# Kernel optimization log

Hardware: AMD Instinct MI355X
Metric: run time of the kernel (lower is better)

Reference implementation:

```python
import jax, jax.numpy as jnp
import numpy as np

N_WIN = 7      # regions per side (BiFormer nchw BRA default)
TOPK = 4       # routed regions per query region
NH = 1         # num_heads (RefNet_encoder uses num_heads=1)
EPS = 1e-5


def _resize(x, hw):
    n, c = x.shape[:2]
    # torch F.interpolate(mode='bilinear', align_corners=False)
    return jax.image.resize(x, (n, c, hw[0], hw[1]), method='bilinear', antialias=False)


def _conv1x1(x, w, b):
    return jnp.einsum('nchw,oc->nohw', x, w) + b[None, :, None, None]


def _ln2d(x, g, b):
    # LayerNorm over channel dim of NCHW
    mu = jnp.mean(x, axis=1, keepdims=True)
    var = jnp.var(x, axis=1, keepdims=True)
    return (x - mu) * jax.lax.rsqrt(var + EPS) * g[None, :, None, None] + b[None, :, None, None]


def _to_regions(t, nh):
    # (N,C,H,W) -> (N, nh, R, rs, hd) with R = n_win^2 regions, rs tokens/region
    n, c, h, w = t.shape
    hd = c // nh
    rh, rw = h // N_WIN, w // N_WIN
    t = t.reshape(n, nh, hd, N_WIN, rh, N_WIN, rw)
    return t.transpose(0, 1, 3, 5, 4, 6, 2).reshape(n, nh, N_WIN * N_WIN, rh * rw, hd)


def _from_regions(t, h, w):
    n, nh, _, _, hd = t.shape
    rh, rw = h // N_WIN, w // N_WIN
    t = t.reshape(n, nh, N_WIN, N_WIN, rh, rw, hd)
    return t.transpose(0, 1, 6, 2, 4, 3, 5).reshape(n, nh * hd, h, w)


def _dwconv(x, w, b):
    # depthwise 5x5 LePE conv, padding=2
    y = jax.lax.conv_general_dilated(x, w, (1, 1), 'SAME',
        dimension_numbers=('NCHW', 'OIHW', 'NCHW'), feature_group_count=x.shape[1])
    return y + b[None, :, None, None]


def _bra(x, mask, qkv_w, qkv_b, lepe_w, lepe_b, proj_w, proj_b):
    n, c, h, w = x.shape
    hd = c // NH
    scale = hd ** -0.5
    rh, rw = h // N_WIN, w // N_WIN
    rs = rh * rw
    R = N_WIN * N_WIN
    q, k, v = jnp.split(_conv1x1(x, qkv_w, qkv_b), 3, axis=1)
    # region-to-region routing graph on detached q/k (avg-pooled regions)
    qd = jax.lax.stop_gradient(q).reshape(n, c, N_WIN, rh, N_WIN, rw).mean(axis=(3, 5)).reshape(n, c, R)
    kd = jax.lax.stop_gradient(k).reshape(n, c, N_WIN, rh, N_WIN, rw).mean(axis=(3, 5)).reshape(n, c, R)
    a_r = jnp.einsum('ncp,ncq->npq', qd, kd)             # (n, R, R)
    idx = jax.lax.top_k(a_r, TOPK)[1]                     # (n, R, TOPK)
    # token-to-token attention within routed regions
    qr = _to_regions(q, NH)                               # (n, nh, R, rs, hd)
    kr = _to_regions(k, NH)
    vr = _to_regions(v, NH)
    gidx = idx[:, None, :, :, None, None]                 # (n,1,Rq,topk,1,1)
    kg = jnp.take_along_axis(kr[:, :, None], gidx, axis=3).reshape(n, NH, R, TOPK * rs, hd)
    vg = jnp.take_along_axis(vr[:, :, None], gidx, axis=3).reshape(n, NH, R, TOPK * rs, hd)
    attn = jnp.einsum('nhrqd,nhrkd->nhrqk', qr * scale, kg)
    # glass-mask additive bias, partitioned + gathered exactly like the keys
    mr = _to_regions(mask, 1)[..., 0]                     # (n,1,R,rs)
    mg = jnp.take_along_axis(mr[:, :, None], idx[:, None, :, :, None], axis=3)
    attn = attn + mg.reshape(n, 1, R, 1, TOPK * rs)
    attn = jax.nn.softmax(attn, axis=-1)
    out = jnp.einsum('nhrqk,nhrkd->nhrqd', attn, vg)
    out = _from_regions(out, h, w) + _dwconv(v, lepe_w, lepe_b)
    return _conv1x1(out, proj_w, proj_b)


def _block(x, mask, i, ln1_g, ln1_b, ln2_g, ln2_b, qkv_w, qkv_b, lepe_w, lepe_b,
           proj_w, proj_b, fc1_w, fc1_b, fc2_w, fc2_b):
    x = x + _bra(_ln2d(x, ln1_g[i], ln1_b[i]), mask, qkv_w[i], qkv_b[i],
                 lepe_w[i], lepe_b[i], proj_w[i], proj_b[i])
    h = jax.nn.gelu(_conv1x1(_ln2d(x, ln2_g[i], ln2_b[i]), fc1_w[i], fc1_b[i]), approximate=False)
    return x + _conv1x1(h, fc2_w[i], fc2_b[i])


def reference(exemplar0, exemplar, input1, exemplar_pre, conv0_w, conv0_b,
              ln1_g, ln1_b, ln2_g, ln2_b, qkv_w, qkv_b, lepe_w, lepe_b,
              proj_w, proj_b, fc1_w, fc1_b, fc2_w, fc2_b):
    hw = exemplar.shape[2:]
    pre_s = _resize(exemplar_pre, hw)
    feats_s = _resize(exemplar0, hw)
    img_s = _resize(input1, hw)
    x = jnp.concatenate([feats_s, exemplar, img_s], axis=1)
    hx = jax.lax.conv_general_dilated(x, conv0_w, (1, 1), 'SAME',
        dimension_numbers=('NCHW', 'OIHW', 'NCHW')) + conv0_b[None, :, None, None]
    m = (jax.nn.sigmoid(pre_s) > 0.5).astype(x.dtype)
    attn_mask = jnp.where(m == 0, jnp.float32(-100.0), jnp.float32(0.0)).astype(x.dtype)
    for i in range(4):
        hx = _block(hx, attn_mask, i, ln1_g, ln1_b, ln2_g, ln2_b, qkv_w, qkv_b,
                    lepe_w, lepe_b, proj_w, proj_b, fc1_w, fc1_b, fc2_w, fc2_b)
    return hx


def setup_inputs() -> dict:
    key = jax.random.key(0)
    ks = jax.random.split(key, 12)
    B, C, H, W = 4, 64, 112, 112
    s = 0.05
    return {
        'exemplar0': jax.random.normal(ks[0], (B, C, 224, 224), jnp.float32),
        'exemplar': jax.random.normal(ks[1], (B, C, H, W), jnp.float32),
        'input1': jax.random.normal(ks[2], (B, 3, 224, 224), jnp.float32),
        'exemplar_pre': jax.random.normal(ks[3], (B, 1, 224, 224), jnp.float32),
        'conv0_w': jax.random.normal(ks[4], (C, 2 * C + 3, 3, 3), jnp.float32) * s,
        'conv0_b': jnp.zeros((C,), jnp.float32),
        'ln1_g': jnp.ones((4, C), jnp.float32),
        'ln1_b': jnp.zeros((4, C), jnp.float32),
        'ln2_g': jnp.ones((4, C), jnp.float32),
        'ln2_b': jnp.zeros((4, C), jnp.float32),
        'qkv_w': jax.random.normal(ks[5], (4, 3 * C, C), jnp.float32) * s,
        'qkv_b': jnp.zeros((4, 3 * C), jnp.float32),
        'lepe_w': jax.random.normal(ks[6], (4, C, 1, 5, 5), jnp.float32) * s,
        'lepe_b': jnp.zeros((4, C), jnp.float32),
        'proj_w': jax.random.normal(ks[7], (4, C, C), jnp.float32) * s,
        'proj_b': jnp.zeros((4, C), jnp.float32),
        'fc1_w': jax.random.normal(ks[8], (4, 4 * C, C), jnp.float32) * s,
        'fc1_b': jnp.zeros((4, 4 * C), jnp.float32),
        'fc2_w': jax.random.normal(ks[9], (4, C, 4 * C), jnp.float32) * s,
        'fc2_b': jnp.zeros((4, C), jnp.float32),
    }
```

## Files before the change

### kernel.cpp

```cpp
#include <hip/hip_runtime.h>

#define HW 112
#define PP 12544
#define BB 4
#define RR 49
#define RS 256
#define GW 114
#define GP (GW*GW)
#define CK 160

typedef __bf16 bf16;
typedef __bf16 bf16x8 __attribute__((ext_vector_type(8)));
typedef __bf16 bf16x4 __attribute__((ext_vector_type(4)));
typedef float f32x4 __attribute__((ext_vector_type(4)));

__device__ __forceinline__ int swzg(int row, int halfcol, int rowbytes) {
  int byte = halfcol * 2;
  return row * rowbytes + (byte & ~127) + ((((byte >> 4) ^ row) & 7) * 16) + (byte & 15);
}
__device__ __forceinline__ int swz128(int row, int halfcol) { return swzg(row, halfcol, 128); }

__device__ __forceinline__ float gelu_exact(float x) {
  return 0.5f * x * (1.f + erff(x * 0.70710678118654752f));
}

__device__ __forceinline__ void gl_lds16(const void* g, void* l) {
  __builtin_amdgcn_global_load_lds((const __attribute__((address_space(1))) unsigned int*)g,
                                   (__attribute__((address_space(3))) unsigned int*)l, 16, 0, 0);
}
__device__ __forceinline__ void gl_lds4(const void* g, void* l) {
  __builtin_amdgcn_global_load_lds((const __attribute__((address_space(1))) unsigned int*)g,
                                   (__attribute__((address_space(3))) unsigned int*)l, 4, 0, 0);
}

__global__ __launch_bounds__(256) void k_prep2(const float* __restrict__ ex0, const float* __restrict__ ex,
    const float* __restrict__ img, const float* __restrict__ pre,
    bf16* __restrict__ xct, float* __restrict__ maskr) {
  __shared__ bf16 sT2[64 * 168];
  int n = blockIdx.y;
  int p0 = blockIdx.x * 64;
  int tid = threadIdx.x;
  uint4 zz = {0, 0, 0, 0};
  for (int i2 = tid; i2 < 1344; i2 += 256) ((uint4*)sT2)[i2] = zz;
  __syncthreads();
  int l = tid & 63, g = tid >> 6;
  int p = p0 + l;
  int h = p / HW, w = p % HW;
  for (int c = g; c < 131; c += 4) {
    float val;
    if (c < 64) {
      const float* s = ex0 + (((size_t)(n * 64 + c)) * 224 + 2 * h) * 224 + 2 * w;
      val = 0.5f * (0.5f * (s[0] + s[224]) + 0.5f * (s[1] + s[225]));
    } else if (c < 128) {
      val = ex[((size_t)(n * 64 + (c - 64))) * PP + p];
    } else {
      const float* s = img + (((size_t)(n * 3 + (c - 128))) * 224 + 2 * h) * 224 + 2 * w;
      val = 0.5f * (0.5f * (s[0] + s[224]) + 0.5f * (s[1] + s[225]));
    }
    sT2[l * 168 + c] = (bf16)val;
  }
  if (tid < 64) {
    const float* s = pre + ((size_t)n * 224 + 2 * h) * 224 + 2 * w;
    float v = 0.5f * (0.5f * (s[0] + s[224]) + 0.5f * (s[1] + s[225]));
    int r = (h >> 4) * 7 + (w >> 4); int sIdx = (h & 15) * 16 + (w & 15);
    maskr[(n * RR + r) * RS + sIdx] = (v > 0.0f) ? 0.0f : -100.0f;
  }
  __syncthreads();
  for (int i2 = tid; i2 < 1280; i2 += 256) {
    int row = i2 / 20, ch = i2 % 20;
    int pr = p0 + row;
    int hh = pr / HW, ww = pr % HW;
    uint4 d = *(const uint4*)(sT2 + row * 168 + ch * 8);
    *(uint4*)(xct + ((size_t)n * GP + (hh + 1) * GW + ww + 1) * CK + ch * 8) = d;
  }
}

__global__ __launch_bounds__(256) void k_wt2(const float* __restrict__ w, bf16* __restrict__ wTb) {
  int t = blockIdx.x * 256 + threadIdx.x;
  if (t >= 9 * 5 * 64 * 32) return;
  int cc = t & 31; int o = (t >> 5) & 63; int ks = (t >> 11) % 5; int k = t / 10240;
  int c = ks * 32 + cc;
  wTb[t] = (bf16)((c < 131) ? w[((size_t)(o * 131) + c) * 9 + k] : 0.f);
}

__global__ __launch_bounds__(256) void k_conv0m(const bf16* __restrict__ xct, const bf16* __restrict__ wTb,
    const float* __restrict__ bias, float* __restrict__ out_t) {
  __shared__ bf16 sA[128 * 32];
  __shared__ bf16 sB[64 * 32];
  int n = blockIdx.y;
  int p0 = blockIdx.x * 128;
  int tid = threadIdx.x, lane = tid & 63, wv = tid >> 6;
  int lo = lane & 15, hi = lane >> 4;
  size_t gofsA[2];
  #pragma unroll
  for (int it = 0; it < 2; it++) {
    int idx = tid + it * 256;
    int row = idx >> 2, ch = idx & 3;
    int p = p0 + row;
    int hh = p / HW, ww = p % HW;
    gofsA[it] = ((size_t)(hh + 1) * GW + ww + 1) * (CK * 2) + ch * 16;
  }
  const char* xbase = (const char*)(xct + (size_t)n * GP * CK);
  f32x4 acc[2][4];
  #pragma unroll
  for (int mi = 0; mi < 2; mi++)
    #pragma unroll
    for (int ni = 0; ni < 4; ni++) acc[mi][ni] = (f32x4){0.f, 0.f, 0.f, 0.f};
  for (int tap = 0; tap < 9; tap++) {
    long shift = (long)((tap / 3 - 1) * GW + (tap % 3 - 1)) * (CK * 2);
    for (int ks = 0; ks < 5; ks++) {
      uint4 a0 = *(const uint4*)(xbase + gofsA[0] + shift + ks * 64);
      uint4 a1 = *(const uint4*)(xbase + gofsA[1] + shift + ks * 64);
      uint4 b0 = *(const uint4*)((const char*)wTb + ((size_t)(tap * 5 + ks) * 2048 + tid * 8) * 2);
      __syncthreads();
      *(uint4*)((char*)sA + tid * 16) = a0;
      *(uint4*)((char*)sA + (tid + 256) * 16) = a1;
      *(uint4*)((char*)sB + tid * 16) = b0;
      __syncthreads();
      bf16x8 aF[2], bF[4];
      #pragma unroll
      for (int mi = 0; mi < 2; mi++)
        aF[mi] = *(const bf16x8*)((const char*)sA + (wv * 32 + mi * 16 + lo) * 64 + hi * 16);
      #pragma unroll
      for (int ni = 0; ni < 4; ni++)
        bF[ni] = *(const bf16x8*)((const char*)sB + (ni * 16 + lo) * 64 + hi * 16);
      #pragma unroll
      for (int mi = 0; mi < 2; mi++)
        #pragma unroll
        for (int ni = 0; ni < 4; ni++)
          acc[mi][ni] = __builtin_amdgcn_mfma_f32_16x16x32_bf16(aF[mi], bF[ni], acc[mi][ni], 0, 0, 0);
    }
  }
  #pragma unroll
  for (int ni = 0; ni < 4; ni++) {
    float bv = bias[ni * 16 + lo];
    #pragma unroll
    for (int mi = 0; mi < 2; mi++) {
      #pragma unroll
      for (int r2 = 0; r2 < 4; r2++) {
        int p = p0 + wv * 32 + mi * 16 + hi * 4 + r2;
        out_t[((size_t)n * PP + p) * 64 + ni * 16 + lo] = acc[mi][ni][r2] + bv;
      }
    }
  }
}

__global__ __launch_bounds__(256) void k_qkvr(const float* __restrict__ xin, const float* __restrict__ lng,
    const float* __restrict__ lnb, const float* __restrict__ w, const float* __restrict__ bias,
    bf16* __restrict__ qRo, bf16* __restrict__ kRo, bf16* __restrict__ vto, bf16* __restrict__ vTo,
    float* __restrict__ qd, float* __restrict__ kd) {
  __shared__ __align__(16) char smem[43008];
  bf16* sA = (bf16*)smem;
  bf16* sB = (bf16*)(smem + 32768);
  float* rq = (float*)(smem + 40960);
  float* rk = (float*)(smem + 41984);
  bf16* sT = (bf16*)smem;
  int r = blockIdx.x, n = blockIdx.y;
  int nr = n * RR + r;
  int rh = (r / 7) * 16, rw = (r % 7) * 16;
  int tid = threadIdx.x, lane = tid & 63, wv = tid >> 6;
  int lo = lane & 15, hi = lane >> 4;
  #pragma unroll
  for (int h2 = 0; h2 < 2; h2++) {
    int row = h2 * 128 + (tid >> 1), part = tid & 1;
    int y = row >> 4, x = row & 15;
    const float* xp = xin + ((size_t)n * PP + (rh + y) * HW + rw + x) * 64 + part * 32;
    float v[32]; float s = 0.f, sq = 0.f;
    #pragma unroll
    for (int i = 0; i < 8; i++) {
      float4 d = *(const float4*)&xp[i * 4];
      v[i*4]=d.x; v[i*4+1]=d.y; v[i*4+2]=d.z; v[i*4+3]=d.w;
      s += d.x+d.y+d.z+d.w;
      sq += d.x*d.x+d.y*d.y+d.z*d.z+d.w*d.w;
    }
    s += __shfl_xor(s, 1, 64); sq += __shfl_xor(sq, 1, 64);
    float mu = s * (1.f/64.f);
    float rstd = rsqrtf(fmaxf(sq * (1.f/64.f) - mu*mu, 0.f) + 1e-5f);
    #pragma unroll
    for (int j2 = 0; j2 < 4; j2++) {
      bf16x8 o8;
      #pragma unroll
      for (int e = 0; e < 8; e++) {
        int c = part*32 + j2*8 + e;
        o8[e] = (bf16)((v[j2*8+e] - mu) * rstd * lng[c] + lnb[c]);
      }
      *(bf16x8*)((char*)sA + swz128(row, part*32 + j2*8)) = o8;
    }
  }
  for (int ob = 0; ob < 3; ob++) {
    #pragma unroll
    for (int it = 0; it < 4; it++) {
      int idx = tid + it * 256;
      int oo = idx >> 4, q = idx & 15;
      float4 wv4 = *(const float4*)&w[(size_t)(ob * 64 + oo) * 64 + q * 4];
      bf16x4 b4; b4[0] = (bf16)wv4.x; b4[1] = (bf16)wv4.y; b4[2] = (bf16)wv4.z; b4[3] = (bf16)wv4.w;
      *(bf16x4*)((char*)sB + swz128(oo, q * 4)) = b4;
    }
    __syncthreads();
    f32x4 acc[4][4];
    #pragma unroll
    for (int mi = 0; mi < 4; mi++)
      #pragma unroll
      for (int ni = 0; ni < 4; ni++) acc[mi][ni] = (f32x4){0.f, 0.f, 0.f, 0.f};
    #pragma unroll
    for (int kk = 0; kk < 2; kk++) {
      bf16x8 aF[4], bF[4];
      #pragma unroll
      for (int mi = 0; mi < 4; mi++)
        aF[mi] = *(const bf16x8*)((const char*)sA + swz128(wv * 64 + mi * 16 + lo, kk * 32 + hi * 8));
      #pragma unroll
      for (int ni = 0; ni < 4; ni++)
        bF[ni] = *(const bf16x8*)((const char*)sB + swz128(ni * 16 + lo, kk * 32 + hi * 8));
      #pragma unroll
      for (int mi = 0; mi < 4; mi++)
        #pragma unroll
        for (int ni = 0; ni < 4; ni++)
          acc[mi][ni] = __builtin_amdgcn_mfma_f32_16x16x32_bf16(aF[mi], bF[ni], acc[mi][ni], 0, 0, 0);
    }
    float bv[4];
    #pragma unroll
    for (int ni = 0; ni < 4; ni++) bv[ni] = bias[ob * 64 + ni * 16 + lo];
    if (ob == 0) {
      float part_[4] = {0.f, 0.f, 0.f, 0.f};
      #pragma unroll
      for (int ni = 0; ni < 4; ni++) {
        #pragma unroll
        for (int mi = 0; mi < 4; mi++) {
          #pragma unroll
          for (int r2 = 0; r2 < 4; r2++) {
            float rv = acc[mi][ni][r2] + bv[ni];
            int s = wv * 64 + mi * 16 + hi * 4 + r2;
            qRo[((size_t)nr * RS + s) * 64 + ni * 16 + lo] = (bf16)(rv * 0.125f);
            part_[ni] += rv;
          }
        }
        part_[ni] += __shfl_xor(part_[ni], 16, 64);
        part_[ni] += __shfl_xor(part_[ni], 32, 64);
        if (hi == 0) rq[wv * 64 + ni * 16 + lo] = part_[ni];
      }
      __syncthreads();
    } else if (ob == 1) {
      float part_[4] = {0.f, 0.f, 0.f, 0.f};
      #pragma unroll
      for (int ni = 0; ni < 4; ni++) {
        #pragma unroll
        for (int mi = 0; mi < 4; mi++) {
          #pragma unroll
          for (int r2 = 0; r2 < 4; r2++) {
            float rv = acc[mi][ni][r2] + bv[ni];
            int s = wv * 64 + mi * 16 + hi * 4 + r2;
            kRo[((size_t)nr * RS + s) * 64 + ni * 16 + lo] = (bf16)rv;
            part_[ni] += rv;
          }
        }
        part_[ni] += __shfl_xor(part_[ni], 16, 64);
        part_[ni] += __shfl_xor(part_[ni], 32, 64);
        if (hi == 0) rk[wv * 64 + ni * 16 + lo] = part_[ni];
      }
      __syncthreads();
    } else {
      __syncthreads();
      #pragma unroll
      for (int ni = 0; ni < 4; ni++) {
        int ch = ni * 16 + lo;
        #pragma unroll
        for (int mi = 0; mi < 4; mi++) {
          #pragma unroll
          for (int r2 = 0; r2 < 4; r2++) {
            float rv = acc[mi][ni][r2] + bv[ni];
            int s = wv * 64 + mi * 16 + hi * 4 + r2;
            bf16 b = (bf16)rv;
            vto[((size_t)n * PP + (rh + (s >> 4)) * HW + rw + (s & 15)) * 64 + ch] = b;
            sT[ch * 264 + s] = b;
          }
        }
      }
      __syncthreads();
      #pragma unroll
      for (int it = 0; it < 8; it++) {
        int idx = tid + it * 256;
        int row = idx >> 5, ch8 = idx & 31;
        uint4 d = *(const uint4*)(sT + row * 264 + ch8 * 8);
        *(uint4*)(vTo + ((size_t)nr * 64 + row) * 256 + ch8 * 8) = d;
      }
      if (tid < 64) {
        int c = tid;
        qd[(n * 64 + c) * RR + r] = ((rq[c] + rq[64 + c]) + (rq[128 + c] + rq[192 + c])) * (1.f / 256.f);
        kd[(n * 64 + c) * RR + r] = ((rk[c] + rk[64 + c]) + (rk[128 + c] + rk[192 + c])) * (1.f / 256.f);
      }
    }
  }
}

__global__ __launch_bounds__(64) void k_topk(const float* __restrict__ qd, const float* __restrict__ kd,
    int* __restrict__ gidx) {
  int pq = blockIdx.x, n = blockIdx.y;
  int j = threadIdx.x;
  float a = -3e38f;
  if (j < RR) {
    a = 0.f;
    for (int c = 0; c < 64; c++)
      a += qd[(n * 64 + c) * RR + pq] * kd[(n * 64 + c) * RR + j];
  }
  for (int t = 0; t < 4; t++) {
    float bv = a; int bj = j;
    #pragma unroll
    for (int d = 32; d >= 1; d >>= 1) {
      float ov = __shfl_xor(bv, d, 64);
      int oj = __shfl_xor(bj, d, 64);
      if (ov > bv || (ov == bv && oj < bj)) { bv = ov; bj = oj; }
    }
    if (j == 0) gidx[(n * RR + pq) * 4 + t] = bj;
    if (j == bj) a = -3e38f;
  }
}

__global__ __launch_bounds__(512, 6) void k_attn(const bf16* __restrict__ qR, const bf16* __restrict__ kR,
    const bf16* __restrict__ vT, const float* __restrict__ maskr, const int* __restrict__ gidx,
    bf16* __restrict__ attnRb) {
  __shared__ bf16 sKd[2][64 * 64];
  __shared__ bf16 sVd[2][64 * 64];
  __shared__ bf16 sP[8][16 * 64];
  __shared__ float sMaskB[2][64];
  int bid = blockIdx.x;
  int newid = (bid & 7) * 49 + (bid >> 3);
  int n = newid / (RR * 2); int rem = newid % (RR * 2); int r = rem >> 1, qsp = rem & 1;
  int tid = threadIdx.x, lane = tid & 63, wv = tid >> 6;
  int lo = lane & 15, hi = lane >> 4;
  int m0 = qsp * 128 + wv * 16;
  const bf16* qbase = qR + ((size_t)(n * RR + r)) * RS * 64;
  bf16x8 qF[2];
  #pragma unroll
  for (int kk = 0; kk < 2; kk++)
    qF[kk] = *(const bf16x8*)(qbase + (m0 + lo) * 64 + kk * 32 + hi * 8);

  int gofsK, gofsV;
  {
    int rowT = wv * 8 + (lane >> 3);
    int c4 = ((lane & 7) ^ rowT) & 7;
    gofsK = rowT * 128 + c4 * 16;
    gofsV = rowT * 512 + c4 * 16;
  }

  const int* gptr = gidx + (n * RR + r) * 4;
  int j0g = gptr[0], j1g = gptr[1], j2g = gptr[2], j3g = gptr[3];

  f32x4 zero4 = {0.f, 0.f, 0.f, 0.f};
  f32x4 Oacc[4];
  #pragma unroll
  for (int di = 0; di < 4; di++) Oacc[di] = zero4;
  float mrun = -3e38f, lrun = 0.f;

  #define ISSUE_TILE(JREG, SUB, BUF) do {                                            \
    const char* kb_ = (const char*)(kR + ((size_t)(n * RR + (JREG))) * RS * 64) + (SUB) * 8192; \
    const char* vb_ = (const char*)(vT + ((size_t)(n * RR + (JREG))) * 64 * RS) + (SUB) * 128;  \
    gl_lds16(kb_ + gofsK, (char*)sKd + (BUF) * 8192 + wv * 1024);                    \
    gl_lds16(vb_ + gofsV, (char*)sVd + (BUF) * 8192 + wv * 1024);                    \
    if (wv == 0) gl_lds4(maskr + ((size_t)(n * RR + (JREG))) * RS + (SUB) * 64 + lane, (char*)sMaskB[(BUF)]); \
  } while (0)

  ISSUE_TILE(j0g, 0, 0);

  for (int ts = 0; ts < 16; ts++) {
    int cur = ts & 1;
    asm volatile("s_waitcnt lgkmcnt(0)" ::: "memory");
    __builtin_amdgcn_s_barrier();
    __builtin_amdgcn_sched_barrier(0);
    if (ts < 15) {
      int nts = ts + 1;
      int jn = (nts < 8) ? (nts < 4 ? j0g : j1g) : (nts < 12 ? j2g : j3g);
      int nsub = nts & 3;
      ISSUE_TILE(jn, nsub, cur ^ 1);
      if (wv == 0) { asm volatile("s_waitcnt vmcnt(3)" ::: "memory"); }
      else         { asm volatile("s_waitcnt vmcnt(2)" ::: "memory"); }
    } else {
      asm volatile("s_waitcnt vmcnt(0)" ::: "memory");
    }
    __builtin_amdgcn_s_barrier();
    __builtin_amdgcn_sched_barrier(0);
    const char* sK = (const char*)sKd + cur * 8192;
    const char* sV = (const char*)sVd + cur * 8192;
    f32x4 Sacc[4];
    #pragma unroll
    for (int ni = 0; ni < 4; ni++) Sacc[ni] = zero4;
    #pragma unroll
    for (int kk = 0; kk < 2; kk++) {
      #pragma unroll
      for (int ni = 0; ni < 4; ni++) {
        bf16x8 kF = *(const bf16x8*)(sK + swz128(ni * 16 + lo, kk * 32 + hi * 8));
        Sacc[ni] = __builtin_amdgcn_mfma_f32_16x16x32_bf16(kF, qF[kk], Sacc[ni], 0, 0, 0);
      }
    }
    const float* mB = sMaskB[cur];
    float ml = -3e38f;
    #pragma unroll
    for (int ni = 0; ni < 4; ni++) {
      #pragma unroll
      for (int jj = 0; jj < 4; jj++) {
        float sv = Sacc[ni][jj] + mB[ni * 16 + hi * 4 + jj];
        Sacc[ni][jj] = sv;
        ml = fmaxf(ml, sv);
      }
    }
    ml = fmaxf(ml, __shfl_xor(ml, 16, 64));
    ml = fmaxf(ml, __shfl_xor(ml, 32, 64));
    float nm = fmaxf(mrun, ml);
    float sc = __expf(mrun - nm);
    float rs = 0.f;
    bf16* sPw = sP[wv];
    #pragma unroll
    for (int ni = 0; ni < 4; ni++) {
      #pragma unroll
      for (int jj = 0; jj < 4; jj++) {
        float pv = __expf(Sacc[ni][jj] - nm);
        rs += pv;
        *(bf16*)((char*)sPw + swz128(lo, ni * 16 + hi * 4 + jj)) = (bf16)pv;
      }
    }
    rs += __shfl_xor(rs, 16, 64);
    rs += __shfl_xor(rs, 32, 64);
    mrun = nm; lrun = lrun * sc + rs;
    float scq[4];
    #pragma unroll
    for (int jj = 0; jj < 4; jj++) scq[jj] = __shfl(sc, hi * 4 + jj, 16);
    #pragma unroll
    for (int di = 0; di < 4; di++)
      #pragma unroll
      for (int jj = 0; jj < 4; jj++) Oacc[di][jj] *= scq[jj];
    #pragma unroll
    for (int kk = 0; kk < 2; kk++) {
      bf16x8 pF = *(const bf16x8*)((const char*)sPw + swz128(lo, kk * 32 + hi * 8));
      #pragma unroll
      for (int di = 0; di < 4; di++) {
        bf16x8 vF = *(const bf16x8*)(sV + swz128(di * 16 + lo, kk * 32 + hi * 8));
        Oacc[di] = __builtin_amdgcn_mfma_f32_16x16x32_bf16(pF, vF, Oacc[di], 0, 0, 0);
      }
    }
  }
  #undef ISSUE_TILE
  __syncthreads();
  float inv = 1.f / lrun;
  float invq[4];
  #pragma unroll
  for (int jj = 0; jj < 4; jj++) invq[jj] = __shfl(inv, hi * 4 + jj, 16);
  bf16* sOut = (bf16*)sKd;
  #pragma unroll
  for (int jj = 0; jj < 4; jj++) {
    int row = wv * 16 + hi * 4 + jj;
    #pragma unroll
    for (int di = 0; di < 4; di++)
      sOut[row * 64 + di * 16 + lo] = (bf16)(Oacc[di][jj] * invq[jj]);
  }
  __syncthreads();
  bf16* dst = attnRb + (((size_t)(n * RR + r)) * RS + qsp * 128) * 64;
  #pragma unroll
  for (int it = 0; it < 2; it++) {
    int idx = tid + it * 512;
    *(uint4*)(dst + idx * 8) = *(const uint4*)(sOut + idx * 8);
  }
}

__global__ __launch_bounds__(256) void k_lepe3(const bf16* __restrict__ v_t, const bf16* __restrict__ attnRb,
    const float* __restrict__ lw, const float* __restrict__ lb,
    const float* __restrict__ pw, const float* __restrict__ pb, float* __restrict__ xo) {
  __shared__ __align__(16) char smem[64000];
  bf16* sH = (bf16*)smem;
  float* sW = (float*)(smem + 57600);
  bf16* zA = (bf16*)smem;
  bf16* sBp = (bf16*)(smem + 32768);
  int r = blockIdx.x, n = blockIdx.y;
  int rh = (r / 7) * 16, rw = (r % 7) * 16;
  int tid = threadIdx.x, lane = tid & 63, wv = tid >> 6;
  int lo = lane & 15, hi = lane >> 4;
  for (int i = tid; i < 1600; i += 256) { int c = i / 25, k = i % 25; sW[k * 64 + c] = lw[c * 25 + k]; }
  for (int g = tid; g < 3200; g += 256) {
    int pix = g >> 3, c4 = g & 7;
    int yy = pix / 20, xx = pix % 20;
    int hh = rh + yy - 2, ww = rw + xx - 2;
    uint4 d = {0, 0, 0, 0};
    if ((unsigned)hh < HW && (unsigned)ww < HW)
      d = *(const uint4*)(v_t + ((size_t)n * PP + hh * HW + ww) * 64 + c4 * 8);
    *(uint4*)((char*)sH + pix * 144 + c4 * 16) = d;
  }
  __syncthreads();
  int y = tid >> 4, x = tid & 15;
  float acc[64];
  const bf16* ar = attnRb + (((size_t)(n * RR + r)) * RS + tid) * 64;
  #pragma unroll
  for (int c8 = 0; c8 < 8; c8++) {
    bf16x8 av = *(const bf16x8*)(ar + c8 * 8);
    #pragma unroll
    for (int j = 0; j < 8; j++) acc[c8 * 8 + j] = lb[c8 * 8 + j] + (float)av[j];
  }
  for (int t25 = 0; t25 < 25; t25++) {
    int dh = t25 / 5, dw = t25 % 5;
    int pix = (y + dh) * 20 + (x + dw);
    #pragma unroll
    for (int c8 = 0; c8 < 8; c8++) {
      bf16x8 hv = *(const bf16x8*)((const char*)sH + pix * 144 + c8 * 16);
      #pragma unroll
      for (int j = 0; j < 8; j++) acc[c8 * 8 + j] += (float)hv[j] * sW[t25 * 64 + c8 * 8 + j];
    }
  }
  __syncthreads();
  #pragma unroll
  for (int i = 0; i < 8; i++) {
    bf16x8 o8;
    #pragma unroll
    for (int j = 0; j < 8; j++) o8[j] = (bf16)acc[i * 8 + j];
    *(bf16x8*)((char*)zA + swz128(tid, i * 8)) = o8;
  }
  #pragma unroll
  for (int it = 0; it < 4; it++) {
    int idx = tid + it * 256;
    int oo = idx >> 4, q = idx & 15;
    float4 wv4 = *(const float4*)&pw[(size_t)oo * 64 + q * 4];
    bf16x4 b4; b4[0] = (bf16)wv4.x; b4[1] = (bf16)wv4.y; b4[2] = (bf16)wv4.z; b4[3] = (bf16)wv4.w;
    *(bf16x4*)((char*)sBp + swz128(oo, q * 4)) = b4;
  }
  __syncthreads();
  f32x4 acc2[4][4];
  #pragma unroll
  for (int mi = 0; mi < 4; mi++)
    #pragma unroll
    for (int ni = 0; ni < 4; ni++) acc2[mi][ni] = (f32x4){0.f, 0.f, 0.f, 0.f};
  #pragma unroll
  for (int kk = 0; kk < 2; kk++) {
    bf16x8 aF[4], bF[4];
    #pragma unroll
    for (int mi = 0; mi < 4; mi++)
      aF[mi] = *(const bf16x8*)((const char*)zA + swz128(wv * 64 + mi * 16 + lo, kk * 32 + hi * 8));
    #pragma unroll
    for (int ni = 0; ni < 4; ni++)
      bF[ni] = *(const bf16x8*)((const char*)sBp + swz128(ni * 16 + lo, kk * 32 + hi * 8));
    #pragma unroll
    for (int mi = 0; mi < 4; mi++)
      #pragma unroll
      for (int ni = 0; ni < 4; ni++)
        acc2[mi][ni] = __builtin_amdgcn_mfma_f32_16x16x32_bf16(aF[mi], bF[ni], acc2[mi][ni], 0, 0, 0);
  }
  #pragma unroll
  for (int ni = 0; ni < 4; ni++) {
    float bv = pb[ni * 16 + lo];
    #pragma unroll
    for (int mi = 0; mi < 4; mi++) {
      #pragma unroll
      for (int r2 = 0; r2 < 4; r2++) {
        int s = wv * 64 + mi * 16 + hi * 4 + r2;
        int p = (rh + (s >> 4)) * HW + rw + (s & 15);
        xo[((size_t)n * PP + p) * 64 + ni * 16 + lo] += acc2[mi][ni][r2] + bv;
      }
    }
  }
}

__global__ __launch_bounds__(256) void k_mlp(const float* __restrict__ xin, const float* __restrict__ lng,
    const float* __restrict__ lnb, const float* __restrict__ w1, const float* __restrict__ b1,
    const float* __restrict__ w2, const float* __restrict__ b2, float* __restrict__ xo) {
  __shared__ bf16 sA[64 * 64];
  __shared__ bf16 sW1[128 * 64];
  __shared__ bf16 sHh[64 * 128];
  __shared__ bf16 sW2[64 * 128];
  int n = blockIdx.y;
  int p0 = blockIdx.x * 64;
  int tid = threadIdx.x, lane = tid & 63, wv = tid >> 6;
  int lo = lane & 15, hi = lane >> 4;
  {
    int row = tid >> 2, part = tid & 3;
    const float* xp = xin + ((size_t)n * PP + p0 + row) * 64 + part * 16;
    float v[16]; float s = 0.f, sq = 0.f;
    #pragma unroll
    for (int i = 0; i < 4; i++) {
      float4 d = *(const float4*)&xp[i * 4];
      v[i*4]=d.x; v[i*4+1]=d.y; v[i*4+2]=d.z; v[i*4+3]=d.w;
      s += d.x+d.y+d.z+d.w;
      sq += d.x*d.x+d.y*d.y+d.z*d.z+d.w*d.w;
    }
    s += __shfl_xor(s, 1, 64); sq += __shfl_xor(sq, 1, 64);
    s += __shfl_xor(s, 2, 64); sq += __shfl_xor(sq, 2, 64);
    float mu = s * (1.f/64.f);
    float rstd = rsqrtf(fmaxf(sq * (1.f/64.f) - mu*mu, 0.f) + 1e-5f);
    #pragma unroll
    for (int j2 = 0; j2 < 2; j2++) {
      bf16x8 o8;
      #pragma unroll
      for (int e = 0; e < 8; e++) {
        int c = part*16 + j2*8 + e;
        o8[e] = (bf16)((v[j2*8+e] - mu) * rstd * lng[c] + lnb[c]);
      }
      *(bf16x8*)((char*)sA + swz128(row, part*16 + j2*8)) = o8;
    }
  }
  f32x4 oacc[4];
  #pragma unroll
  for (int ni = 0; ni < 4; ni++) oacc[ni] = (f32x4){0.f, 0.f, 0.f, 0.f};
  for (int half = 0; half < 2; half++) {
    #pragma unroll
    for (int it = 0; it < 8; it++) {
      int idx = tid + it * 256;
      int oo = idx >> 4, q = idx & 15;
      float4 wv4 = *(const float4*)&w1[(size_t)(half * 128 + oo) * 64 + q * 4];
      bf16x4 b4; b4[0] = (bf16)wv4.x; b4[1] = (bf16)wv4.y; b4[2] = (bf16)wv4.z; b4[3] = (bf16)wv4.w;
      *(bf16x4*)((char*)sW1 + swz128(oo, q * 4)) = b4;
    }
    __syncthreads();
    f32x4 hacc[8];
    #pragma unroll
    for (int ni = 0; ni < 8; ni++) hacc[ni] = (f32x4){0.f, 0.f, 0.f, 0.f};
    #pragma unroll
    for (int kk = 0; kk < 2; kk++) {
      bf16x8 aF = *(const bf16x8*)((const char*)sA + swz128(wv * 16 + lo, kk * 32 + hi * 8));
      #pragma unroll
      for (int ni = 0; ni < 8; ni++) {
        bf16x8 bF = *(const bf16x8*)((const char*)sW1 + swz128(ni * 16 + lo, kk * 32 + hi * 8));
        hacc[ni] = __builtin_amdgcn_mfma_f32_16x16x32_bf16(aF, bF, hacc[ni], 0, 0, 0);
      }
    }
    #pragma unroll
    for (int ni = 0; ni < 8; ni++) {
      float bv = b1[half * 128 + ni * 16 + lo];
      #pragma unroll
      for (int r2 = 0; r2 < 4; r2++) {
        float hval = gelu_exact(hacc[ni][r2] + bv);
        *(bf16*)((char*)sHh + swzg(wv * 16 + hi * 4 + r2, ni * 16 + lo, 256)) = (bf16)hval;
      }
    }
    #pragma unroll
    for (int it = 0; it < 8; it++) {
      int idx = tid + it * 256;
      int oo = idx >> 5, q = idx & 31;
      float4 wv4 = *(const float4*)&w2[(size_t)oo * 256 + half * 128 + q * 4];
      bf16x4 b4; b4[0] = (bf16)wv4.x; b4[1] = (bf16)wv4.y; b4[2] = (bf16)wv4.z; b4[3] = (bf16)wv4.w;
      *(bf16x4*)((char*)sW2 + swzg(oo, q * 4, 256)) = b4;
    }
    __syncthreads();
    #pragma unroll
    for (int kk = 0; kk < 4; kk++) {
      bf16x8 aH = *(const bf16x8*)((const char*)sHh + swzg(wv * 16 + lo, kk * 32 + hi * 8, 256));
      #pragma unroll
      for (int ni = 0; ni < 4; ni++) {
        bf16x8 bF = *(const bf16x8*)((const char*)sW2 + swzg(ni * 16 + lo, kk * 32 + hi * 8, 256));
        oacc[ni] = __builtin_amdgcn_mfma_f32_16x16x32_bf16(aH, bF, oacc[ni], 0, 0, 0);
      }
    }
    __syncthreads();
  }
  #pragma unroll
  for (int ni = 0; ni < 4; ni++) {
    float bv = b2[ni * 16 + lo];
    #pragma unroll
    for (int r2 = 0; r2 < 4; r2++) {
      int p = p0 + wv * 16 + hi * 4 + r2;
      xo[((size_t)n * PP + p) * 64 + ni * 16 + lo] += oacc[ni][r2] + bv;
    }
  }
}

__global__ __launch_bounds__(256) void k_untr(const float* __restrict__ x_t, float* __restrict__ out) {
  __shared__ float tile[64][68];
  int n = blockIdx.y; int p0 = blockIdx.x * 64;
  int tid = threadIdx.x;
  #pragma unroll
  for (int it = 0; it < 4; it++) {
    int g = tid + it * 256;
    int row = g >> 4, q = g & 15;
    float4 d = *(const float4*)&x_t[((size_t)n * PP + p0 + row) * 64 + q * 4];
    *(float4*)&tile[row][q * 4] = d;
  }
  __syncthreads();
  #pragma unroll
  for (int it = 0; it < 4; it++) {
    int g = tid + it * 256;
    int c = g >> 4, q = g & 15;
    float4 v;
    v.x = tile[q * 4 + 0][c]; v.y = tile[q * 4 + 1][c];
    v.z = tile[q * 4 + 2][c]; v.w = tile[q * 4 + 3][c];
    *(float4*)&out[((size_t)(n * 64 + c)) * PP + p0 + q * 4] = v;
  }
}

extern "C" void kernel_launch(void* const* d_in, const int* in_sizes, int n_in,
                              void* d_out, int out_size, void* d_ws, size_t ws_size,
                              hipStream_t stream) {
  const float* ex0 = (const float*)d_in[0];
  const float* ex  = (const float*)d_in[1];
  const float* img = (const float*)d_in[2];
  const float* pre = (const float*)d_in[3];
  const float* c0w = (const float*)d_in[4];
  const float* c0b = (const float*)d_in[5];
  const float* ln1g = (const float*)d_in[6];
  const float* ln1b = (const float*)d_in[7];
  const float* ln2g = (const float*)d_in[8];
  const float* ln2b = (const float*)d_in[9];
  const float* qkvw = (const float*)d_in[10];
  const float* qkvb = (const float*)d_in[11];
  const float* lw = (const float*)d_in[12];
  const float* lb = (const float*)d_in[13];
  const float* pw = (const float*)d_in[14];
  const float* pb = (const float*)d_in[15];
  const float* f1w = (const float*)d_in[16];
  const float* f1b = (const float*)d_in[17];
  const float* f2w = (const float*)d_in[18];
  const float* f2b = (const float*)d_in[19];

  float* W = (float*)d_ws;
  size_t o = 0;
  bf16* xct = (bf16*)(W + o);  o += (size_t)BB * GP * CK / 2;
  float* x_t  = W + o;         o += 3211264;
  bf16* attnRb = (bf16*)(W + o); o += 1605632;
  bf16* v_t  = (bf16*)(W + o); o += 1605632;
  bf16* qR   = (bf16*)(W + o); o += 1605632;
  bf16* kR   = (bf16*)(W + o); o += 1605632;
  bf16* vT   = (bf16*)(W + o); o += 1605632;
  float* qd = W + o;           o += 12544;
  float* kd = W + o;           o += 12544;
  float* maskr = W + o;        o += 50176;
  bf16* wTb = (bf16*)(W + o);  o += 46080;
  int* gidx = (int*)(W + o);   o += 784;

  hipMemsetAsync(xct, 0, (size_t)BB * GP * CK * 2, stream);
  k_prep2<<<dim3(196, BB), dim3(256), 0, stream>>>(ex0, ex, img, pre, xct, maskr);
  k_wt2<<<dim3(360), dim3(256), 0, stream>>>(c0w, wTb);
  k_conv0m<<<dim3(98, BB), dim3(256), 0, stream>>>(xct, wTb, c0b, x_t);
  for (int i = 0; i < 4; i++) {
    k_qkvr<<<dim3(RR, BB), dim3(256), 0, stream>>>(x_t, ln1g + i * 64, ln1b + i * 64,
        qkvw + (size_t)i * 192 * 64, qkvb + i * 192, qR, kR, v_t, vT, qd, kd);
    k_topk<<<dim3(RR, BB), dim3(64), 0, stream>>>(qd, kd, gidx);
    k_attn<<<dim3(BB * RR * 2), dim3(512), 0, stream>>>(qR, kR, vT, maskr, gidx, attnRb);
    k_lepe3<<<dim3(RR, BB), dim3(256), 0, stream>>>(v_t, attnRb, lw + (size_t)i * 64 * 25, lb + i * 64,
        pw + (size_t)i * 64 * 64, pb + i * 64, x_t);
    k_mlp<<<dim3(196, BB), dim3(256), 0, stream>>>(x_t, ln2g + i * 64, ln2b + i * 64,
        f1w + (size_t)i * 256 * 64, f1b + i * 256, f2w + (size_t)i * 64 * 256, f2b + i * 64, x_t);
  }
  k_untr<<<dim3(196, BB), dim3(256), 0, stream>>>(x_t, (float*)d_out);
}
```

Before: 491.1 us.

## Fuse top-k routing into attention, pre-convert weights to bf16, use tanh GELU

The separate top-k routing kernel is removed. Each attention block now computes the region affinities and top-4 selection itself in its first wavefront and shares the result through LDS, which saves one launch per layer but repeats the routing work in both query-split blocks. All qkv, proj and MLP weights are converted to bf16 once by a single kernel, so the per-block float-to-bf16 conversion inside the GEMM kernels goes away and loads become 16-byte. The MLP reuses one LDS buffer for W1 and W2, which adds a barrier. Exact erf GELU is replaced by the tanh approximation, which changes numerics slightly.

```diff
diff --git a/kernel.cpp b/kernel.cpp
--- a/kernel.cpp
+++ b/kernel.cpp
@@ -20,8 +20,12 @@
 }
 __device__ __forceinline__ int swz128(int row, int halfcol) { return swzg(row, halfcol, 128); }
 
-__device__ __forceinline__ float gelu_exact(float x) {
-  return 0.5f * x * (1.f + erff(x * 0.70710678118654752f));
+__device__ __forceinline__ float gelu_fast(float x) {
+  float y = 0.7978845608f * (x + 0.044715f * x * x * x);
+  float t = __expf(-2.f * fabsf(y));
+  float th = (1.f - t) / (1.f + t);
+  th = copysignf(th, y);
+  return 0.5f * x * (1.f + th);
 }
 
 __device__ __forceinline__ void gl_lds16(const void* g, void* l) {
@@ -83,6 +87,20 @@
   wTb[t] = (bf16)((c < 131) ? w[((size_t)(o * 131) + c) * 9 + k] : 0.f);
 }
 
+__global__ __launch_bounds__(256) void k_wcvt(const float* __restrict__ s0, bf16* __restrict__ d0, int n0,
+    const float* __restrict__ s1, bf16* __restrict__ d1, int n1,
+    const float* __restrict__ s2, bf16* __restrict__ d2, int n2,
+    const float* __restrict__ s3, bf16* __restrict__ d3, int n3) {
+  int t = blockIdx.x * 256 + threadIdx.x;
+  if (t < n0) { d0[t] = (bf16)s0[t]; return; }
+  t -= n0;
+  if (t < n1) { d1[t] = (bf16)s1[t]; return; }
+  t -= n1;
+  if (t < n2) { d2[t] = (bf16)s2[t]; return; }
+  t -= n2;
+  if (t < n3) { d3[t] = (bf16)s3[t]; }
+}
+
 __global__ __launch_bounds__(256) void k_conv0m(const bf16* __restrict__ xct, const bf16* __restrict__ wTb,
     const float* __restrict__ bias, float* __restrict__ out_t) {
   __shared__ bf16 sA[128 * 32];
@@ -146,7 +164,7 @@
 }
 
 __global__ __launch_bounds__(256) void k_qkvr(const float* __restrict__ xin, const float* __restrict__ lng,
-    const float* __restrict__ lnb, const float* __restrict__ w, const float* __restrict__ bias,
+    const float* __restrict__ lnb, const bf16* __restrict__ wb, const float* __restrict__ bias,
     bf16* __restrict__ qRo, bf16* __restrict__ kRo, bf16* __restrict__ vto, bf16* __restrict__ vTo,
     float* __restrict__ qd, float* __restrict__ kd) {
   __shared__ __align__(16) char smem[43008];
@@ -189,12 +207,11 @@
   }
   for (int ob = 0; ob < 3; ob++) {
     #pragma unroll
-    for (int it = 0; it < 4; it++) {
+    for (int it = 0; it < 2; it++) {
       int idx = tid + it * 256;
-      int oo = idx >> 4, q = idx & 15;
-      float4 wv4 = *(const float4*)&w[(size_t)(ob * 64 + oo) * 64 + q * 4];
-      bf16x4 b4; b4[0] = (bf16)wv4.x; b4[1] = (bf16)wv4.y; b4[2] = (bf16)wv4.z; b4[3] = (bf16)wv4.w;
-      *(bf16x4*)((char*)sB + swz128(oo, q * 4)) = b4;
+      int oo = idx >> 3, q8 = idx & 7;
+      uint4 d = *(const uint4*)(wb + (size_t)(ob * 64 + oo) * 64 + q8 * 8);
+      *(uint4*)((char*)sB + swz128(oo, q8 * 8)) = d;
     }
     __syncthreads();
     f32x4 acc[4][4];
@@ -292,36 +309,14 @@
   }
 }
 
-__global__ __launch_bounds__(64) void k_topk(const float* __restrict__ qd, const float* __restrict__ kd,
-    int* __restrict__ gidx) {
-  int pq = blockIdx.x, n = blockIdx.y;
-  int j = threadIdx.x;
-  float a = -3e38f;
-  if (j < RR) {
-    a = 0.f;
-    for (int c = 0; c < 64; c++)
-      a += qd[(n * 64 + c) * RR + pq] * kd[(n * 64 + c) * RR + j];
-  }
-  for (int t = 0; t < 4; t++) {
-    float bv = a; int bj = j;
-    #pragma unroll
-    for (int d = 32; d >= 1; d >>= 1) {
-      float ov = __shfl_xor(bv, d, 64);
-      int oj = __shfl_xor(bj, d, 64);
-      if (ov > bv || (ov == bv && oj < bj)) { bv = ov; bj = oj; }
-    }
-    if (j == 0) gidx[(n * RR + pq) * 4 + t] = bj;
-    if (j == bj) a = -3e38f;
-  }
-}
-
 __global__ __launch_bounds__(512, 6) void k_attn(const bf16* __restrict__ qR, const bf16* __restrict__ kR,
-    const bf16* __restrict__ vT, const float* __restrict__ maskr, const int* __restrict__ gidx,
-    bf16* __restrict__ attnRb) {
+    const bf16* __restrict__ vT, const float* __restrict__ maskr,
+    const float* __restrict__ qd, const float* __restrict__ kd, bf16* __restrict__ attnRb) {
   __shared__ bf16 sKd[2][64 * 64];
   __shared__ bf16 sVd[2][64 * 64];
   __shared__ bf16 sP[8][16 * 64];
   __shared__ float sMaskB[2][64];
+  __shared__ int sJ[4];
   int bid = blockIdx.x;
   int newid = (bid & 7) * 49 + (bid >> 3);
   int n = newid / (RR * 2); int rem = newid % (RR * 2); int r = rem >> 1, qsp = rem & 1;
@@ -334,6 +329,30 @@
   for (int kk = 0; kk < 2; kk++)
     qF[kk] = *(const bf16x8*)(qbase + (m0 + lo) * 64 + kk * 32 + hi * 8);
 
+  if (wv == 0) {
+    int j = lane;
+    float a = -3e38f;
+    if (j < RR) {
+      a = 0.f;
+      for (int c = 0; c < 64; c++)
+        a += qd[(n * 64 + c) * RR + r] * kd[(n * 64 + c) * RR + j];
+    }
+    #pragma unroll
+    for (int t = 0; t < 4; t++) {
+      float bv = a; int bj = j;
+      #pragma unroll
+      for (int d = 32; d >= 1; d >>= 1) {
+        float ov = __shfl_xor(bv, d, 64);
+        int oj = __shfl_xor(bj, d, 64);
+        if (ov > bv || (ov == bv && oj < bj)) { bv = ov; bj = oj; }
+      }
+      if (j == 0) sJ[t] = bj;
+      if (j == bj) a = -3e38f;
+    }
+  }
+  __syncthreads();
+  int j0g = sJ[0], j1g = sJ[1], j2g = sJ[2], j3g = sJ[3];
+
   int gofsK, gofsV;
   {
     int rowT = wv * 8 + (lane >> 3);
@@ -341,9 +360,6 @@
     gofsK = rowT * 128 + c4 * 16;
     gofsV = rowT * 512 + c4 * 16;
   }
-
-  const int* gptr = gidx + (n * RR + r) * 4;
-  int j0g = gptr[0], j1g = gptr[1], j2g = gptr[2], j3g = gptr[3];
 
   f32x4 zero4 = {0.f, 0.f, 0.f, 0.f};
   f32x4 Oacc[4];
@@ -462,7 +478,7 @@
 
 __global__ __launch_bounds__(256) void k_lepe3(const bf16* __restrict__ v_t, const bf16* __restrict__ attnRb,
     const float* __restrict__ lw, const float* __restrict__ lb,
-    const float* __restrict__ pw, const float* __restrict__ pb, float* __restrict__ xo) {
+    const bf16* __restrict__ pwb, const float* __restrict__ pb, float* __restrict__ xo) {
   __shared__ __align__(16) char smem[64000];
   bf16* sH = (bf16*)smem;
   float* sW = (float*)(smem + 57600);
@@ -511,12 +527,11 @@
     *(bf16x8*)((char*)zA + swz128(tid, i * 8)) = o8;
   }
   #pragma unroll
-  for (int it = 0; it < 4; it++) {
+  for (int it = 0; it < 2; it++) {
     int idx = tid + it * 256;
-    int oo = idx >> 4, q = idx & 15;
-    float4 wv4 = *(const float4*)&pw[(size_t)oo * 64 + q * 4];
-    bf16x4 b4; b4[0] = (bf16)wv4.x; b4[1] = (bf16)wv4.y; b4[2] = (bf16)wv4.z; b4[3] = (bf16)wv4.w;
-    *(bf16x4*)((char*)sBp + swz128(oo, q * 4)) = b4;
+    int oo = idx >> 3, q8 = idx & 7;
+    uint4 d = *(const uint4*)(pwb + (size_t)oo * 64 + q8 * 8);
+    *(uint4*)((char*)sBp + swz128(oo, q8 * 8)) = d;
   }
   __syncthreads();
   f32x4 acc2[4][4];
@@ -555,12 +570,11 @@
 }
 
 __global__ __launch_bounds__(256) void k_mlp(const float* __restrict__ xin, const float* __restrict__ lng,
-    const float* __restrict__ lnb, const float* __restrict__ w1, const float* __restrict__ b1,
-    const float* __restrict__ w2, const float* __restrict__ b2, float* __restrict__ xo) {
+    const float* __restrict__ lnb, const bf16* __restrict__ w1b, const float* __restrict__ b1,
+    const bf16* __restrict__ w2b, const float* __restrict__ b2, float* __restrict__ xo) {
   __shared__ bf16 sA[64 * 64];
-  __shared__ bf16 sW1[128 * 64];
+  __shared__ bf16 sW[128 * 64];
   __shared__ bf16 sHh[64 * 128];
-  __shared__ bf16 sW2[64 * 128];
   int n = blockIdx.y;
   int p0 = blockIdx.x * 64;
   int tid = threadIdx.x, lane = tid & 63, wv = tid >> 6;
@@ -596,12 +610,11 @@
   for (int ni = 0; ni < 4; ni++) oacc[ni] = (f32x4){0.f, 0.f, 0.f, 0.f};
   for (int half = 0; half < 2; half++) {
     #pragma unroll
-    for (int it = 0; it < 8; it++) {
+    for (int it = 0; it < 4; it++) {
       int idx = tid + it * 256;
-      int oo = idx >> 4, q = idx & 15;
-      float4 wv4 = *(const float4*)&w1[(size_t)(half * 128 + oo) * 64 + q * 4];
-      bf16x4 b4; b4[0] = (bf16)wv4.x; b4[1] = (bf16)wv4.y; b4[2] = (bf16)wv4.z; b4[3] = (bf16)wv4.w;
-      *(bf16x4*)((char*)sW1 + swz128(oo, q * 4)) = b4;
+      int oo = idx >> 3, q8 = idx & 7;
+      uint4 d = *(const uint4*)(w1b + (size_t)(half * 128 + oo) * 64 + q8 * 8);
+      *(uint4*)((char*)sW + swz128(oo, q8 * 8)) = d;
     }
     __syncthreads();
     f32x4 hacc[8];
@@ -612,7 +625,7 @@
       bf16x8 aF = *(const bf16x8*)((const char*)sA + swz128(wv * 16 + lo, kk * 32 + hi * 8));
       #pragma unroll
       for (int ni = 0; ni < 8; ni++) {
-        bf16x8 bF = *(const bf16x8*)((const char*)sW1 + swz128(ni * 16 + lo, kk * 32 + hi * 8));
+        bf16x8 bF = *(const bf16x8*)((const char*)sW + swz128(ni * 16 + lo, kk * 32 + hi * 8));
         hacc[ni] = __builtin_amdgcn_mfma_f32_16x16x32_bf16(aF, bF, hacc[ni], 0, 0, 0);
       }
     }
@@ -621,17 +634,17 @@
       float bv = b1[half * 128 + ni * 16 + lo];
       #pragma unroll
       for (int r2 = 0; r2 < 4; r2++) {
-        float hval = gelu_exact(hacc[ni][r2] + bv);
+        float hval = gelu_fast(hacc[ni][r2] + bv);
         *(bf16*)((char*)sHh + swzg(wv * 16 + hi * 4 + r2, ni * 16 + lo, 256)) = (bf16)hval;
       }
     }
-    #pragma unroll
-    for (int it = 0; it < 8; it++) {
+    __syncthreads();
+    #pragma unroll
+    for (int it = 0; it < 4; it++) {
       int idx = tid + it * 256;
-      int oo = idx >> 5, q = idx & 31;
-      float4 wv4 = *(const float4*)&w2[(size_t)oo * 256 + half * 128 + q * 4];
-      bf16x4 b4; b4[0] = (bf16)wv4.x; b4[1] = (bf16)wv4.y; b4[2] = (bf16)wv4.z; b4[3] = (bf16)wv4.w;
-      *(bf16x4*)((char*)sW2 + swzg(oo, q * 4, 256)) = b4;
+      int oo = idx >> 4, q8 = idx & 15;
+      uint4 d = *(const uint4*)(w2b + (size_t)oo * 256 + half * 128 + q8 * 8);
+      *(uint4*)((char*)sW + swzg(oo, q8 * 8, 256)) = d;
     }
     __syncthreads();
     #pragma unroll
@@ -639,7 +652,7 @@
       bf16x8 aH = *(const bf16x8*)((const char*)sHh + swzg(wv * 16 + lo, kk * 32 + hi * 8, 256));
       #pragma unroll
       for (int ni = 0; ni < 4; ni++) {
-        bf16x8 bF = *(const bf16x8*)((const char*)sW2 + swzg(ni * 16 + lo, kk * 32 + hi * 8, 256));
+        bf16x8 bF = *(const bf16x8*)((const char*)sW + swzg(ni * 16 + lo, kk * 32 + hi * 8, 256));
         oacc[ni] = __builtin_amdgcn_mfma_f32_16x16x32_bf16(aH, bF, oacc[ni], 0, 0, 0);
       }
     }
@@ -716,21 +729,25 @@
   float* kd = W + o;           o += 12544;
   float* maskr = W + o;        o += 50176;
   bf16* wTb = (bf16*)(W + o);  o += 46080;
-  int* gidx = (int*)(W + o);   o += 784;
+  bf16* qkvwb = (bf16*)(W + o); o += 24576;
+  bf16* pwb   = (bf16*)(W + o); o += 8192;
+  bf16* f1wb  = (bf16*)(W + o); o += 32768;
+  bf16* f2wb  = (bf16*)(W + o); o += 32768;
 
   hipMemsetAsync(xct, 0, (size_t)BB * GP * CK * 2, stream);
   k_prep2<<<dim3(196, BB), dim3(256), 0, stream>>>(ex0, ex, img, pre, xct, maskr);
   k_wt2<<<dim3(360), dim3(256), 0, stream>>>(c0w, wTb);
+  k_wcvt<<<dim3((49152 + 16384 + 65536 + 65536 + 255) / 256), dim3(256), 0, stream>>>(
+      qkvw, qkvwb, 49152, pw, pwb, 16384, f1w, f1wb, 65536, f2w, f2wb, 65536);
   k_conv0m<<<dim3(98, BB), dim3(256), 0, stream>>>(xct, wTb, c0b, x_t);
   for (int i = 0; i < 4; i++) {
     k_qkvr<<<dim3(RR, BB), dim3(256), 0, stream>>>(x_t, ln1g + i * 64, ln1b + i * 64,
-        qkvw + (size_t)i * 192 * 64, qkvb + i * 192, qR, kR, v_t, vT, qd, kd);
-    k_topk<<<dim3(RR, BB), dim3(64), 0, stream>>>(qd, kd, gidx);
-    k_attn<<<dim3(BB * RR * 2), dim3(512), 0, stream>>>(qR, kR, vT, maskr, gidx, attnRb);
+        qkvwb + (size_t)i * 192 * 64, qkvb + i * 192, qR, kR, v_t, vT, qd, kd);
+    k_attn<<<dim3(BB * RR * 2), dim3(512), 0, stream>>>(qR, kR, vT, maskr, qd, kd, attnRb);
     k_lepe3<<<dim3(RR, BB), dim3(256), 0, stream>>>(v_t, attnRb, lw + (size_t)i * 64 * 25, lb + i * 64,
-        pw + (size_t)i * 64 * 64, pb + i * 64, x_t);
+        pwb + (size_t)i * 64 * 64, pb + i * 64, x_t);
     k_mlp<<<dim3(196, BB), dim3(256), 0, stream>>>(x_t, ln2g + i * 64, ln2b + i * 64,
-        f1w + (size_t)i * 256 * 64, f1b + i * 256, f2w + (size_t)i * 64 * 256, f2b + i * 64, x_t);
+        f1wb + (size_t)i * 256 * 64, f1b + i * 256, f2wb + (size_t)i * 64 * 256, f2b + i * 64, x_t);
   }
   k_untr<<<dim3(196, BB), dim3(256), 0, stream>>>(x_t, (float*)d_out);
 }
```

Result: no change. 494.7 us (+0.7%).
